# Kernel optimization log

Measured on AMD Instinct MI355X. Metric: run time of the kernel, lower is better.

The kernel has to match this reference:

```python
import jax, jax.numpy as jnp
import numpy as np
import math

B, S, D = 2, 2048, 2048
H, KV, HD = 32, 8, 64
G = H // KV  # 4
BASE = 10000.0


def _rope_tables(seq_len, dtype):
    inv_freq = 1.0 / (BASE ** (jnp.arange(0, HD, 2, dtype=jnp.float32) / HD))
    t = jnp.arange(seq_len, dtype=jnp.float32)
    freqs = jnp.outer(t, inv_freq)               # [S, HD/2]
    emb = jnp.concatenate([freqs, freqs], -1)     # [S, HD]
    return jnp.cos(emb).astype(dtype), jnp.sin(emb).astype(dtype)


def _rotate_half(x):
    x1, x2 = x[..., : HD // 2], x[..., HD // 2 :]
    return jnp.concatenate([-x2, x1], axis=-1)


def setup_inputs() -> dict:
    key = jax.random.key(0)
    ks = jax.random.split(key, 5)
    s = 0.02
    return {
        "hidden_states": jax.random.normal(ks[0], (B, S, D), jnp.float32),
        "Wq": jax.random.normal(ks[1], (D, H * HD), jnp.float32) * s,
        "Wk": jax.random.normal(ks[2], (D, KV * HD), jnp.float32) * s,
        "Wv": jax.random.normal(ks[3], (D, KV * HD), jnp.float32) * s,
        "Wo": jax.random.normal(ks[4], (D, D), jnp.float32) * s,
    }


def reference(hidden_states, Wq, Wk, Wv, Wo):
    b, s, _ = hidden_states.shape
    q = (hidden_states @ Wq).reshape(b, s, H, HD).transpose(0, 2, 1, 3)   # [B,H,S,HD]
    k = (hidden_states @ Wk).reshape(b, s, KV, HD).transpose(0, 2, 1, 3)  # [B,KV,S,HD]
    v = (hidden_states @ Wv).reshape(b, s, KV, HD).transpose(0, 2, 1, 3)

    cos, sin = _rope_tables(s, hidden_states.dtype)  # [S, HD]
    cos = cos[None, None]
    sin = sin[None, None]
    q = q * cos + _rotate_half(q) * sin
    k = k * cos + _rotate_half(k) * sin

    # GQA: repeat kv heads to match query heads
    k = jnp.repeat(k, G, axis=1)  # [B,H,S,HD]
    v = jnp.repeat(v, G, axis=1)

    scores = jnp.einsum("bhqd,bhkd->bhqk", q, k) / math.sqrt(HD)
    causal = jnp.triu(jnp.full((s, s), float("-inf"), dtype=scores.dtype), k=1)
    scores = scores + causal
    attn = jax.nn.softmax(scores, axis=-1)
    out = jnp.einsum("bhqk,bhkd->bhqd", attn, v)          # [B,H,S,HD]
    out = out.transpose(0, 2, 1, 3).reshape(b, s, H * HD)  # [B,S,D]
    return out @ Wo
```

## Files before the change

### kernel.cpp

```cpp
#include <hip/hip_runtime.h>
#include <hip/hip_bf16.h>

#define BATCH  2
#define SEQ    2048
#define DMODEL 2048
#define NHEADS 32
#define NKV    8
#define HDIM   64
#define ROWS   (BATCH * SEQ)
#define NQKV   3072

typedef __attribute__((ext_vector_type(8))) short bf16x8;
typedef __attribute__((ext_vector_type(4))) float floatx4;

__device__ __forceinline__ float b2f(unsigned short u) {
    union { unsigned int i; float f; } x; x.i = ((unsigned int)u) << 16; return x.f;
}
__device__ __forceinline__ unsigned short f2b(float f) {
    union { float f; unsigned int i; } x; x.f = f;
    unsigned int r = x.i + 0x7fffu + ((x.i >> 16) & 1u);
    return (unsigned short)(r >> 16);
}
__device__ __forceinline__ unsigned int pkbf(float a, float b) {
    union { __hip_bfloat162 h; unsigned int u; } x;
    x.h = __float22bfloat162_rn(make_float2(a, b));
    return x.u;
}

#define GLD16(g, l) __builtin_amdgcn_global_load_lds( \
    (const __attribute__((address_space(1))) unsigned int*)(g), \
    (__attribute__((address_space(3))) unsigned int*)(l), 16, 0, 0)

template <bool BF16_OUT>
__global__ __launch_bounds__(256) void mfma_gemm(const unsigned short* __restrict__ A,
                                                 const unsigned short* __restrict__ Bt,
                                                 void* __restrict__ Cout,
                                                 int M, int N, int K) {
    __shared__ unsigned short As[3][128 * 32];
    __shared__ unsigned short Bs[3][128 * 32];

    const int tid  = threadIdx.x;
    const int wave = tid >> 6;
    const int lane = tid & 63;
    const int m0 = blockIdx.y * 128;
    const int n0 = blockIdx.x * 128;
    const int wr0 = (wave >> 1) * 64;
    const int wc0 = (wave & 1) * 64;

    const int srow = wave * 32 + (lane >> 2);
    const int skc  = (lane & 3) * 8;
    const unsigned short* Ap0 = A  + (size_t)(m0 + srow) * K + skc;
    const unsigned short* Ap1 = Ap0 + (size_t)16 * K;
    const unsigned short* Bp0 = Bt + (size_t)(n0 + srow) * K + skc;
    const unsigned short* Bp1 = Bp0 + (size_t)16 * K;

    const int fr = lane & 15;
    const int fk = (lane >> 4) * 8;

    floatx4 acc[4][4];
    #pragma unroll
    for (int r = 0; r < 4; ++r)
        #pragma unroll
        for (int c = 0; c < 4; ++c)
            #pragma unroll
            for (int g = 0; g < 4; ++g) acc[r][c][g] = 0.f;

    const int NT = K >> 5;

    auto stage = [&](int t, int buf) {
        unsigned short* Ab = &As[buf][wave * 1024];
        unsigned short* Bb = &Bs[buf][wave * 1024];
        const int k0 = t * 32;
        GLD16(Ap0 + k0, Ab);
        GLD16(Ap1 + k0, Ab + 512);
        GLD16(Bp0 + k0, Bb);
        GLD16(Bp1 + k0, Bb + 512);
    };

    stage(0, 0);
    stage(1, 1);
    asm volatile("s_waitcnt vmcnt(4)" ::: "memory");
    __builtin_amdgcn_s_barrier();
    __builtin_amdgcn_sched_barrier(0);

    int cur = 0, nx2 = 2;
    for (int T = 0; T < NT; ++T) {
        if (T + 2 < NT) stage(T + 2, nx2);

        const unsigned short* Asb = &As[cur][0];
        const unsigned short* Bsb = &Bs[cur][0];
        bf16x8 af[4], bfr[4];
        #pragma unroll
        for (int r = 0; r < 4; ++r)
            af[r] = *(const bf16x8*)&Asb[(wr0 + r * 16 + fr) * 32 + fk];
        #pragma unroll
        for (int c = 0; c < 4; ++c)
            bfr[c] = *(const bf16x8*)&Bsb[(wc0 + c * 16 + fr) * 32 + fk];
        #pragma unroll
        for (int r = 0; r < 4; ++r)
            #pragma unroll
            for (int c = 0; c < 4; ++c)
                acc[r][c] = __builtin_amdgcn_mfma_f32_16x16x32_bf16(af[r], bfr[c], acc[r][c], 0, 0, 0);

        if (T + 1 < NT) {
            if (T + 2 < NT)
                asm volatile("s_waitcnt vmcnt(4)" ::: "memory");
            else
                asm volatile("s_waitcnt vmcnt(0)" ::: "memory");
            __builtin_amdgcn_s_barrier();
            __builtin_amdgcn_sched_barrier(0);
        }
        cur = (cur == 2) ? 0 : cur + 1;
        nx2 = (nx2 == 2) ? 0 : nx2 + 1;
    }

    const int erow = (lane >> 4) * 4;
    const int ecol = lane & 15;
    #pragma unroll
    for (int r = 0; r < 4; ++r)
        #pragma unroll
        for (int c = 0; c < 4; ++c)
            #pragma unroll
            for (int g = 0; g < 4; ++g) {
                int row = m0 + wr0 + r * 16 + erow + g;
                int col = n0 + wc0 + c * 16 + ecol;
                if (BF16_OUT)
                    ((unsigned short*)Cout)[(size_t)row * N + col] = f2b(acc[r][c][g]);
                else
                    ((float*)Cout)[(size_t)row * N + col] = acc[r][c][g];
            }
}

__global__ __launch_bounds__(256) void transpose_cast_all(const float* __restrict__ Wq,
                                                          const float* __restrict__ Wk,
                                                          const float* __restrict__ Wv,
                                                          const float* __restrict__ Wo,
                                                          unsigned short* __restrict__ Wt,
                                                          unsigned short* __restrict__ Wot) {
    __shared__ float t[32][33];
    int bx = blockIdx.x;
    const float* src; unsigned short* dst; int N, nb;
    if (bx < 64)      { src = Wq; dst = Wt;                          N = 2048; nb = bx; }
    else if (bx < 80) { src = Wk; dst = Wt + (size_t)2048 * DMODEL;  N = 512;  nb = bx - 64; }
    else if (bx < 96) { src = Wv; dst = Wt + (size_t)2560 * DMODEL;  N = 512;  nb = bx - 80; }
    else              { src = Wo; dst = Wot;                         N = 2048; nb = bx - 96; }
    const int n0 = nb * 32, k0 = blockIdx.y * 32;
    const int tx = threadIdx.x & 31, ty = threadIdx.x >> 5;
    #pragma unroll
    for (int i = 0; i < 32; i += 8)
        t[ty + i][tx] = src[(size_t)(k0 + ty + i) * N + n0 + tx];
    __syncthreads();
    #pragma unroll
    for (int i = 0; i < 32; i += 8)
        dst[(size_t)(n0 + ty + i) * DMODEL + k0 + tx] = f2b(t[tx][ty + i]);
}

__global__ void cast_f32_to_bf16(const float* __restrict__ src,
                                 unsigned short* __restrict__ dst, int n) {
    int i = (blockIdx.x * 256 + threadIdx.x) * 8;
    if (i >= n) return;
    float4 a = *(const float4*)(src + i);
    float4 b = *(const float4*)(src + i + 4);
    uint4 o;
    o.x = pkbf(a.x, a.y); o.y = pkbf(a.z, a.w);
    o.z = pkbf(b.x, b.y); o.w = pkbf(b.z, b.w);
    *(uint4*)(dst + i) = o;
}

__global__ void rope_all(unsigned short* __restrict__ buf) {
    int idx = blockIdx.x * blockDim.x + threadIdx.x;
    int i   = idx & 31;
    int tmp = idx >> 5;
    int hh  = tmp % 40;
    int row = tmp / 40;
    if (row >= ROWS) return;
    float scale = (hh < 32) ? 0.125f : 1.0f;
    int t = row & (SEQ - 1);
    float inv_freq = powf(10000.0f, -(float)i * (1.0f / 32.0f));
    float ang = (float)t * inv_freq;
    float s, c;
    sincosf(ang, &s, &c);
    unsigned short* p = buf + (size_t)row * NQKV + hh * 64 + i;
    float x1 = b2f(p[0]), x2 = b2f(p[32]);
    p[0]  = f2b((x1 * c - x2 * s) * scale);
    p[32] = f2b((x2 * c + x1 * s) * scale);
}

__global__ __launch_bounds__(256, 5) void attn_mfma(const unsigned short* __restrict__ QKV,
                                                    unsigned short* __restrict__ Ctx) {
    __shared__ unsigned short Ks[64][72];
    __shared__ unsigned short Vts[64][72];
    __shared__ unsigned short Ps[4][16][72];

    const int tid  = threadIdx.x;
    const int wave = tid >> 6;
    const int lane = tid & 63;
    const int px = blockIdx.x;
    const int h  = blockIdx.y;
    const int b  = blockIdx.z;
    const int kvh = h >> 2;

    const int fr = lane & 15;
    const int fg = lane >> 4;
    const size_t base = (size_t)(b * SEQ) * NQKV;

    const int krow = tid >> 2, kc0 = (tid & 3) * 16;
    const int vp2 = tid & 31, vh0 = (tid >> 5) * 8;
    const unsigned short* kbase = QKV + base + (size_t)krow * NQKV + 2048 + kvh * HDIM + kc0;
    const unsigned short* vbase = QKV + base + (size_t)(2 * vp2) * NQKV + 2560 + kvh * HDIM + vh0;

    #pragma unroll 1
    for (int t = 0; t < 2; ++t) {
        const int qb = (t == 0) ? (31 - px) : px;
        const int wbase = qb * 64 + wave * 16;

        bf16x8 qf[2];
        #pragma unroll
        for (int ks = 0; ks < 2; ++ks)
            qf[ks] = *(const bf16x8*)(QKV + base + (size_t)(wbase + fr) * NQKV
                                      + h * HDIM + ks * 32 + fg * 8);

        float l = 0.f;
        floatx4 acc[4];
        #pragma unroll
        for (int j2 = 0; j2 < 4; ++j2)
            #pragma unroll
            for (int g = 0; g < 4; ++g) acc[j2][g] = 0.f;

        const int nkb = qb + 1;

        bf16x8 kr0 = *(const bf16x8*)kbase;
        bf16x8 kr1 = *(const bf16x8*)(kbase + 8);
        bf16x8 v0  = *(const bf16x8*)vbase;
        bf16x8 v1  = *(const bf16x8*)(vbase + NQKV);

        for (int kb = 0; kb < nkb; ++kb) {
            __syncthreads();
            *(bf16x8*)&Ks[krow][kc0]     = kr0;
            *(bf16x8*)&Ks[krow][kc0 + 8] = kr1;
            #pragma unroll
            for (int j = 0; j < 8; ++j) {
                unsigned int w = (unsigned int)(unsigned short)v0[j]
                               | ((unsigned int)(unsigned short)v1[j] << 16);
                *(unsigned int*)&Vts[vh0 + j][2 * vp2] = w;
            }
            {
                int nx = (kb + 1 < nkb) ? kb + 1 : kb;
                const unsigned short* kp = kbase + (size_t)(nx * 64) * NQKV;
                const unsigned short* vp = vbase + (size_t)(nx * 64) * NQKV;
                kr0 = *(const bf16x8*)kp;
                kr1 = *(const bf16x8*)(kp + 8);
                v0  = *(const bf16x8*)vp;
                v1  = *(const bf16x8*)(vp + NQKV);
            }
            __syncthreads();

            const bool skip = (kb * 64 > wbase + 15);
            if (!skip) {
                const bool needMask = (kb * 64 + 63 > wbase);

                floatx4 sc[4];
                #pragma unroll
                for (int j = 0; j < 4; ++j)
                    #pragma unroll
                    for (int g = 0; g < 4; ++g) sc[j][g] = 0.f;
                __builtin_amdgcn_s_setprio(1);
                #pragma unroll
                for (int ks = 0; ks < 2; ++ks) {
                    #pragma unroll
                    for (int j = 0; j < 4; ++j) {
                        bf16x8 kf = *(const bf16x8*)&Ks[j * 16 + fr][ks * 32 + fg * 8];
                        sc[j] = __builtin_amdgcn_mfma_f32_16x16x32_bf16(kf, qf[ks], sc[j], 0, 0, 0);
                    }
                }
                __builtin_amdgcn_s_setprio(0);

                if (needMask) {
                    int qi = wbase + fr;
                    #pragma unroll
                    for (int j = 0; j < 4; ++j)
                        #pragma unroll
                        for (int g = 0; g < 4; ++g) {
                            int kj = kb * 64 + j * 16 + fg * 4 + g;
                            if (kj > qi) sc[j][g] = -1e30f;
                        }
                }

                #pragma unroll
                for (int j = 0; j < 4; ++j) {
                    #pragma unroll
                    for (int g = 0; g < 4; ++g) {
                        float e = __expf(sc[j][g]);
                        sc[j][g] = e;
                        l += e;
                    }
                    uint2 w;
                    w.x = pkbf(sc[j][0], sc[j][1]);
                    w.y = pkbf(sc[j][2], sc[j][3]);
                    *(uint2*)&Ps[wave][fr][j * 16 + fg * 4] = w;
                }

                __builtin_amdgcn_s_setprio(1);
                #pragma unroll
                for (int ks = 0; ks < 2; ++ks) {
                    bf16x8 pf = *(const bf16x8*)&Ps[wave][fr][ks * 32 + fg * 8];
                    #pragma unroll
                    for (int j2 = 0; j2 < 4; ++j2) {
                        bf16x8 vf = *(const bf16x8*)&Vts[j2 * 16 + fr][ks * 32 + fg * 8];
                        acc[j2] = __builtin_amdgcn_mfma_f32_16x16x32_bf16(vf, pf, acc[j2], 0, 0, 0);
                    }
                }
                __builtin_amdgcn_s_setprio(0);
            }
        }

        {
            float lt = l;
            lt += __shfl_xor(lt, 16);
            lt += __shfl_xor(lt, 32);
            float inv = 1.0f / lt;
            int q = wbase + fr;
            unsigned short* cp = Ctx + (size_t)(b * SEQ + q) * DMODEL + h * HDIM;
            #pragma unroll
            for (int j2 = 0; j2 < 4; ++j2) {
                uint2 w;
                w.x = pkbf(acc[j2][0] * inv, acc[j2][1] * inv);
                w.y = pkbf(acc[j2][2] * inv, acc[j2][3] * inv);
                *(uint2*)(cp + j2 * 16 + fg * 4) = w;
            }
        }
    }
}

extern "C" void kernel_launch(void* const* d_in, const int* in_sizes, int n_in,
                              void* d_out, int out_size, void* d_ws, size_t ws_size,
                              hipStream_t stream) {
    const float* X  = (const float*)d_in[0];
    const float* Wq = (const float*)d_in[1];
    const float* Wk = (const float*)d_in[2];
    const float* Wv = (const float*)d_in[3];
    const float* Wo = (const float*)d_in[4];
    float* out = (float*)d_out;

    unsigned short* Xb   = (unsigned short*)d_ws;
    unsigned short* Wt   = Xb + (size_t)ROWS * DMODEL;
    unsigned short* Wot  = Wt + (size_t)NQKV * DMODEL;
    unsigned short* QKVb = Wot + (size_t)DMODEL * DMODEL;
    unsigned short* Ctxb = QKVb + (size_t)ROWS * NQKV;

    cast_f32_to_bf16<<<(ROWS * DMODEL) / (8 * 256), 256, 0, stream>>>(X, Xb, ROWS * DMODEL);
    transpose_cast_all<<<dim3(160, 64), 256, 0, stream>>>(Wq, Wk, Wv, Wo, Wt, Wot);

    mfma_gemm<true><<<dim3(NQKV / 128, ROWS / 128), 256, 0, stream>>>(Xb, Wt, QKVb, ROWS, NQKV, DMODEL);

    rope_all<<<(ROWS * 40 * 32) / 256, 256, 0, stream>>>(QKVb);

    attn_mfma<<<dim3(SEQ / 128, NHEADS, BATCH), 256, 0, stream>>>(QKVb, Ctxb);

    mfma_gemm<false><<<dim3(DMODEL / 128, ROWS / 128), 256, 0, stream>>>(Ctxb, Wot, out, ROWS, DMODEL, DMODEL);
}
```

Baseline: 320.6 us.

## Fuse RoPE into QKV GEMM epilogue and load K fragments directly to registers

Applies rotary embedding and query scaling inside the QKV GEMM epilogue on the fp32 accumulators, which removes the separate rope_all kernel and its read-modify-write pass over the QKV buffer. This works because each wave's 64-column tile holds one full head, so the paired halves are acc[c] and acc[c+2]. The attention kernel also drops the K shared-memory tile and loads K MFMA fragments straight from global memory into registers, prefetching the next block after the score MFMAs. The occupancy hint is lowered from 5 to 4 to leave room for the extra registers. The trade-off is more register pressure, less coalesced K loads, and extra sincos work in the GEMM epilogue.

```diff
diff --git a/kernel.cpp b/kernel.cpp
--- a/kernel.cpp
+++ b/kernel.cpp
@@ -31,7 +31,7 @@
     (const __attribute__((address_space(1))) unsigned int*)(g), \
     (__attribute__((address_space(3))) unsigned int*)(l), 16, 0, 0)
 
-template <bool BF16_OUT>
+template <bool BF16_OUT, bool DO_ROPE>
 __global__ __launch_bounds__(256) void mfma_gemm(const unsigned short* __restrict__ A,
                                                  const unsigned short* __restrict__ Bt,
                                                  void* __restrict__ Cout,
@@ -116,6 +116,31 @@
 
     const int erow = (lane >> 4) * 4;
     const int ecol = lane & 15;
+
+    if (DO_ROPE) {
+        const int colb = n0 + wc0;
+        if (colb < 2560) {
+            const float scale = (colb < 2048) ? 0.125f : 1.0f;
+            const float inv0 = powf(10000.0f, -(float)ecol        * (1.0f / 32.0f));
+            const float inv1 = powf(10000.0f, -(float)(ecol + 16) * (1.0f / 32.0f));
+            #pragma unroll
+            for (int r = 0; r < 4; ++r)
+                #pragma unroll
+                for (int g = 0; g < 4; ++g) {
+                    float t = (float)((m0 + wr0 + r * 16 + erow + g) & (SEQ - 1));
+                    float s0, c0, s1, c1;
+                    sincosf(t * inv0, &s0, &c0);
+                    sincosf(t * inv1, &s1, &c1);
+                    float a0 = acc[r][0][g], a2 = acc[r][2][g];
+                    acc[r][0][g] = (a0 * c0 - a2 * s0) * scale;
+                    acc[r][2][g] = (a2 * c0 + a0 * s0) * scale;
+                    float a1 = acc[r][1][g], a3 = acc[r][3][g];
+                    acc[r][1][g] = (a1 * c1 - a3 * s1) * scale;
+                    acc[r][3][g] = (a3 * c1 + a1 * s1) * scale;
+                }
+        }
+    }
+
     #pragma unroll
     for (int r = 0; r < 4; ++r)
         #pragma unroll
@@ -167,28 +192,8 @@
     *(uint4*)(dst + i) = o;
 }
 
-__global__ void rope_all(unsigned short* __restrict__ buf) {
-    int idx = blockIdx.x * blockDim.x + threadIdx.x;
-    int i   = idx & 31;
-    int tmp = idx >> 5;
-    int hh  = tmp % 40;
-    int row = tmp / 40;
-    if (row >= ROWS) return;
-    float scale = (hh < 32) ? 0.125f : 1.0f;
-    int t = row & (SEQ - 1);
-    float inv_freq = powf(10000.0f, -(float)i * (1.0f / 32.0f));
-    float ang = (float)t * inv_freq;
-    float s, c;
-    sincosf(ang, &s, &c);
-    unsigned short* p = buf + (size_t)row * NQKV + hh * 64 + i;
-    float x1 = b2f(p[0]), x2 = b2f(p[32]);
-    p[0]  = f2b((x1 * c - x2 * s) * scale);
-    p[32] = f2b((x2 * c + x1 * s) * scale);
-}
-
-__global__ __launch_bounds__(256, 5) void attn_mfma(const unsigned short* __restrict__ QKV,
+__global__ __launch_bounds__(256, 4) void attn_mfma(const unsigned short* __restrict__ QKV,
                                                     unsigned short* __restrict__ Ctx) {
-    __shared__ unsigned short Ks[64][72];
     __shared__ unsigned short Vts[64][72];
     __shared__ unsigned short Ps[4][16][72];
 
@@ -204,10 +209,9 @@
     const int fg = lane >> 4;
     const size_t base = (size_t)(b * SEQ) * NQKV;
 
-    const int krow = tid >> 2, kc0 = (tid & 3) * 16;
     const int vp2 = tid & 31, vh0 = (tid >> 5) * 8;
-    const unsigned short* kbase = QKV + base + (size_t)krow * NQKV + 2048 + kvh * HDIM + kc0;
     const unsigned short* vbase = QKV + base + (size_t)(2 * vp2) * NQKV + 2560 + kvh * HDIM + vh0;
+    const unsigned short* kfrag0 = QKV + base + (size_t)fr * NQKV + 2048 + kvh * HDIM + fg * 8;
 
     #pragma unroll 1
     for (int t = 0; t < 2; ++t) {
@@ -229,15 +233,17 @@
 
         const int nkb = qb + 1;
 
-        bf16x8 kr0 = *(const bf16x8*)kbase;
-        bf16x8 kr1 = *(const bf16x8*)(kbase + 8);
-        bf16x8 v0  = *(const bf16x8*)vbase;
-        bf16x8 v1  = *(const bf16x8*)(vbase + NQKV);
+        bf16x8 kf[2][4];
+        #pragma unroll
+        for (int ks = 0; ks < 2; ++ks)
+            #pragma unroll
+            for (int j = 0; j < 4; ++j)
+                kf[ks][j] = *(const bf16x8*)(kfrag0 + (size_t)(j * 16) * NQKV + ks * 32);
+        bf16x8 v0 = *(const bf16x8*)vbase;
+        bf16x8 v1 = *(const bf16x8*)(vbase + NQKV);
 
         for (int kb = 0; kb < nkb; ++kb) {
             __syncthreads();
-            *(bf16x8*)&Ks[krow][kc0]     = kr0;
-            *(bf16x8*)&Ks[krow][kc0 + 8] = kr1;
             #pragma unroll
             for (int j = 0; j < 8; ++j) {
                 unsigned int w = (unsigned int)(unsigned short)v0[j]
@@ -246,35 +252,41 @@
             }
             {
                 int nx = (kb + 1 < nkb) ? kb + 1 : kb;
-                const unsigned short* kp = kbase + (size_t)(nx * 64) * NQKV;
                 const unsigned short* vp = vbase + (size_t)(nx * 64) * NQKV;
-                kr0 = *(const bf16x8*)kp;
-                kr1 = *(const bf16x8*)(kp + 8);
-                v0  = *(const bf16x8*)vp;
-                v1  = *(const bf16x8*)(vp + NQKV);
+                v0 = *(const bf16x8*)vp;
+                v1 = *(const bf16x8*)(vp + NQKV);
             }
             __syncthreads();
 
             const bool skip = (kb * 64 > wbase + 15);
+            const bool needMask = (kb * 64 + 63 > wbase);
+
+            floatx4 sc[4];
             if (!skip) {
-                const bool needMask = (kb * 64 + 63 > wbase);
-
-                floatx4 sc[4];
                 #pragma unroll
                 for (int j = 0; j < 4; ++j)
                     #pragma unroll
                     for (int g = 0; g < 4; ++g) sc[j][g] = 0.f;
                 __builtin_amdgcn_s_setprio(1);
                 #pragma unroll
-                for (int ks = 0; ks < 2; ++ks) {
-                    #pragma unroll
-                    for (int j = 0; j < 4; ++j) {
-                        bf16x8 kf = *(const bf16x8*)&Ks[j * 16 + fr][ks * 32 + fg * 8];
-                        sc[j] = __builtin_amdgcn_mfma_f32_16x16x32_bf16(kf, qf[ks], sc[j], 0, 0, 0);
-                    }
-                }
+                for (int ks = 0; ks < 2; ++ks)
+                    #pragma unroll
+                    for (int j = 0; j < 4; ++j)
+                        sc[j] = __builtin_amdgcn_mfma_f32_16x16x32_bf16(kf[ks][j], qf[ks], sc[j], 0, 0, 0);
                 __builtin_amdgcn_s_setprio(0);
-
+            }
+
+            {
+                int nx = (kb + 1 < nkb) ? kb + 1 : kb;
+                const unsigned short* kp = kfrag0 + (size_t)(nx * 64) * NQKV;
+                #pragma unroll
+                for (int ks = 0; ks < 2; ++ks)
+                    #pragma unroll
+                    for (int j = 0; j < 4; ++j)
+                        kf[ks][j] = *(const bf16x8*)(kp + (size_t)(j * 16) * NQKV + ks * 32);
+            }
+
+            if (!skip) {
                 if (needMask) {
                     int qi = wbase + fr;
                     #pragma unroll
@@ -351,11 +363,9 @@
     cast_f32_to_bf16<<<(ROWS * DMODEL) / (8 * 256), 256, 0, stream>>>(X, Xb, ROWS * DMODEL);
     transpose_cast_all<<<dim3(160, 64), 256, 0, stream>>>(Wq, Wk, Wv, Wo, Wt, Wot);
 
-    mfma_gemm<true><<<dim3(NQKV / 128, ROWS / 128), 256, 0, stream>>>(Xb, Wt, QKVb, ROWS, NQKV, DMODEL);
-
-    rope_all<<<(ROWS * 40 * 32) / 256, 256, 0, stream>>>(QKVb);
+    mfma_gemm<true, true><<<dim3(NQKV / 128, ROWS / 128), 256, 0, stream>>>(Xb, Wt, QKVb, ROWS, NQKV, DMODEL);
 
     attn_mfma<<<dim3(SEQ / 128, NHEADS, BATCH), 256, 0, stream>>>(QKVb, Ctxb);
 
-    mfma_gemm<false><<<dim3(DMODEL / 128, ROWS / 128), 256, 0, stream>>>(Ctxb, Wot, out, ROWS, DMODEL, DMODEL);
-}
+    mfma_gemm<false, false><<<dim3(DMODEL / 128, ROWS / 128), 256, 0, stream>>>(Ctxb, Wot, out, ROWS, DMODEL, DMODEL);
+}
```

Measured after the change: 463.5 us. 44.6% more time.

## Fuse RoPE into QKV GEMM epilogue and double-buffer attention K/V tiles

Applied to the files above, without the earlier changes.

Removes the separate RoPE kernel by applying the rotation and Q scaling inside the QKV GEMM epilogue, using a precomputed cos/sin table built by a small new kernel. This avoids a full read-modify-write pass over the Q/K buffer and one launch. Separately, the attention kernel double-buffers its K and V shared tiles so the barrier at the top of each key block is removed. The extra shared memory lowers the occupancy hint from 5 to 3 blocks per CU.

```diff
diff --git a/kernel.cpp b/kernel.cpp
--- a/kernel.cpp
+++ b/kernel.cpp
@@ -31,10 +31,20 @@
     (const __attribute__((address_space(1))) unsigned int*)(g), \
     (__attribute__((address_space(3))) unsigned int*)(l), 16, 0, 0)
 
-template <bool BF16_OUT>
+__global__ void rope_table(float2* __restrict__ tab) {
+    int idx = blockIdx.x * 256 + threadIdx.x;
+    int i = idx & 31, t = idx >> 5;
+    float inv = powf(10000.0f, -(float)i * (1.0f / 32.0f));
+    float s, c;
+    sincosf((float)t * inv, &s, &c);
+    tab[idx] = make_float2(c, s);
+}
+
+template <bool BF16_OUT, bool DO_ROPE>
 __global__ __launch_bounds__(256) void mfma_gemm(const unsigned short* __restrict__ A,
                                                  const unsigned short* __restrict__ Bt,
                                                  void* __restrict__ Cout,
+                                                 const float2* __restrict__ rtab,
                                                  int M, int N, int K) {
     __shared__ unsigned short As[3][128 * 32];
     __shared__ unsigned short Bs[3][128 * 32];
@@ -116,6 +126,28 @@
 
     const int erow = (lane >> 4) * 4;
     const int ecol = lane & 15;
+
+    if (DO_ROPE) {
+        const int colb = n0 + wc0;
+        if (colb < 2560) {
+            const float scale = (colb < 2048) ? 0.125f : 1.0f;
+            #pragma unroll
+            for (int r = 0; r < 4; ++r)
+                #pragma unroll
+                for (int g = 0; g < 4; ++g) {
+                    int t = (m0 + wr0 + r * 16 + erow + g) & (SEQ - 1);
+                    float2 cs0 = rtab[t * 32 + ecol];
+                    float2 cs1 = rtab[t * 32 + ecol + 16];
+                    float a0 = acc[r][0][g], a2 = acc[r][2][g];
+                    acc[r][0][g] = (a0 * cs0.x - a2 * cs0.y) * scale;
+                    acc[r][2][g] = (a2 * cs0.x + a0 * cs0.y) * scale;
+                    float a1 = acc[r][1][g], a3 = acc[r][3][g];
+                    acc[r][1][g] = (a1 * cs1.x - a3 * cs1.y) * scale;
+                    acc[r][3][g] = (a3 * cs1.x + a1 * cs1.y) * scale;
+                }
+        }
+    }
+
     #pragma unroll
     for (int r = 0; r < 4; ++r)
         #pragma unroll
@@ -167,29 +199,10 @@
     *(uint4*)(dst + i) = o;
 }
 
-__global__ void rope_all(unsigned short* __restrict__ buf) {
-    int idx = blockIdx.x * blockDim.x + threadIdx.x;
-    int i   = idx & 31;
-    int tmp = idx >> 5;
-    int hh  = tmp % 40;
-    int row = tmp / 40;
-    if (row >= ROWS) return;
-    float scale = (hh < 32) ? 0.125f : 1.0f;
-    int t = row & (SEQ - 1);
-    float inv_freq = powf(10000.0f, -(float)i * (1.0f / 32.0f));
-    float ang = (float)t * inv_freq;
-    float s, c;
-    sincosf(ang, &s, &c);
-    unsigned short* p = buf + (size_t)row * NQKV + hh * 64 + i;
-    float x1 = b2f(p[0]), x2 = b2f(p[32]);
-    p[0]  = f2b((x1 * c - x2 * s) * scale);
-    p[32] = f2b((x2 * c + x1 * s) * scale);
-}
-
-__global__ __launch_bounds__(256, 5) void attn_mfma(const unsigned short* __restrict__ QKV,
+__global__ __launch_bounds__(256, 3) void attn_mfma(const unsigned short* __restrict__ QKV,
                                                     unsigned short* __restrict__ Ctx) {
-    __shared__ unsigned short Ks[64][72];
-    __shared__ unsigned short Vts[64][72];
+    __shared__ unsigned short Ks[2][64][72];
+    __shared__ unsigned short Vts[2][64][72];
     __shared__ unsigned short Ps[4][16][72];
 
     const int tid  = threadIdx.x;
@@ -235,14 +248,14 @@
         bf16x8 v1  = *(const bf16x8*)(vbase + NQKV);
 
         for (int kb = 0; kb < nkb; ++kb) {
-            __syncthreads();
-            *(bf16x8*)&Ks[krow][kc0]     = kr0;
-            *(bf16x8*)&Ks[krow][kc0 + 8] = kr1;
+            const int pb = kb & 1;
+            *(bf16x8*)&Ks[pb][krow][kc0]     = kr0;
+            *(bf16x8*)&Ks[pb][krow][kc0 + 8] = kr1;
             #pragma unroll
             for (int j = 0; j < 8; ++j) {
                 unsigned int w = (unsigned int)(unsigned short)v0[j]
                                | ((unsigned int)(unsigned short)v1[j] << 16);
-                *(unsigned int*)&Vts[vh0 + j][2 * vp2] = w;
+                *(unsigned int*)&Vts[pb][vh0 + j][2 * vp2] = w;
             }
             {
                 int nx = (kb + 1 < nkb) ? kb + 1 : kb;
@@ -269,7 +282,7 @@
                 for (int ks = 0; ks < 2; ++ks) {
                     #pragma unroll
                     for (int j = 0; j < 4; ++j) {
-                        bf16x8 kf = *(const bf16x8*)&Ks[j * 16 + fr][ks * 32 + fg * 8];
+                        bf16x8 kf = *(const bf16x8*)&Ks[pb][j * 16 + fr][ks * 32 + fg * 8];
                         sc[j] = __builtin_amdgcn_mfma_f32_16x16x32_bf16(kf, qf[ks], sc[j], 0, 0, 0);
                     }
                 }
@@ -306,13 +319,14 @@
                     bf16x8 pf = *(const bf16x8*)&Ps[wave][fr][ks * 32 + fg * 8];
                     #pragma unroll
                     for (int j2 = 0; j2 < 4; ++j2) {
-                        bf16x8 vf = *(const bf16x8*)&Vts[j2 * 16 + fr][ks * 32 + fg * 8];
+                        bf16x8 vf = *(const bf16x8*)&Vts[pb][j2 * 16 + fr][ks * 32 + fg * 8];
                         acc[j2] = __builtin_amdgcn_mfma_f32_16x16x32_bf16(vf, pf, acc[j2], 0, 0, 0);
                     }
                 }
                 __builtin_amdgcn_s_setprio(0);
             }
         }
+        __syncthreads();
 
         {
             float lt = l;
@@ -347,15 +361,15 @@
     unsigned short* Wot  = Wt + (size_t)NQKV * DMODEL;
     unsigned short* QKVb = Wot + (size_t)DMODEL * DMODEL;
     unsigned short* Ctxb = QKVb + (size_t)ROWS * NQKV;
-
+    float2* Rtab = (float2*)(Ctxb + (size_t)ROWS * DMODEL);
+
+    rope_table<<<256, 256, 0, stream>>>(Rtab);
     cast_f32_to_bf16<<<(ROWS * DMODEL) / (8 * 256), 256, 0, stream>>>(X, Xb, ROWS * DMODEL);
     transpose_cast_all<<<dim3(160, 64), 256, 0, stream>>>(Wq, Wk, Wv, Wo, Wt, Wot);
 
-    mfma_gemm<true><<<dim3(NQKV / 128, ROWS / 128), 256, 0, stream>>>(Xb, Wt, QKVb, ROWS, NQKV, DMODEL);
-
-    rope_all<<<(ROWS * 40 * 32) / 256, 256, 0, stream>>>(QKVb);
+    mfma_gemm<true, true><<<dim3(NQKV / 128, ROWS / 128), 256, 0, stream>>>(Xb, Wt, QKVb, Rtab, ROWS, NQKV, DMODEL);
 
     attn_mfma<<<dim3(SEQ / 128, NHEADS, BATCH), 256, 0, stream>>>(QKVb, Ctxb);
 
-    mfma_gemm<false><<<dim3(DMODEL / 128, ROWS / 128), 256, 0, stream>>>(Ctxb, Wot, out, ROWS, DMODEL, DMODEL);
-}
+    mfma_gemm<false, false><<<dim3(DMODEL / 128, ROWS / 128), 256, 0, stream>>>(Ctxb, Wot, out, Rtab, ROWS, DMODEL, DMODEL);
+}
```

Result: slower. 336.6 us (+5.0%).
